# Kernel optimization log

Measured on AMD Instinct MI355X. Metric: run time of the kernel, lower is better.

## Reference

```python
import jax, jax.numpy as jnp
import numpy as np

H = 256  # rnn hidden size

def _rnn_dir(x, wih, whh, bih, bhh):
    # x: [B,T,D] -> outputs [B,T,H]; h_t = tanh(x_t Wih^T + bih + h_{t-1} Whh^T + bhh)
    xproj = jnp.einsum('btd,hd->bth', x, wih) + bih + bhh  # precompute input projection
    def step(h, xp):
        h = jnp.tanh(xp + h @ whh.T)
        return h, h
    h0 = jnp.zeros((x.shape[0], whh.shape[0]), x.dtype)
    _, ys = jax.lax.scan(step, h0, jnp.swapaxes(xproj, 0, 1))
    return jnp.swapaxes(ys, 0, 1)

def _birnn(x, wif, whf, bif, bhf, wib, whb, bib, bhb):
    fwd = _rnn_dir(x, wif, whf, bif, bhf)
    bwd = _rnn_dir(x[:, ::-1, :], wib, whb, bib, bhb)[:, ::-1, :]
    return jnp.concatenate([fwd, bwd], axis=-1)

def setup_inputs() -> dict:
    key = jax.random.key(0)
    ks = jax.random.split(key, 24)
    B, T, V, E = 64, 512, 131072, 128
    s = 0.05
    emb = jax.random.normal(ks[0], (V, E), jnp.float32) * s
    emb = emb.at[0].set(0.0)  # padding_idx=0
    def W(k, shp):
        return jax.random.normal(k, shp, jnp.float32) * s
    inp = {
        'x': jax.random.randint(ks[1], (B, T), 0, V),
        'emb': emb,
        'r1_wif': W(ks[2], (H, E)), 'r1_whf': W(ks[3], (H, H)),
        'r1_bif': W(ks[4], (H,)), 'r1_bhf': W(ks[5], (H,)),
        'r1_wib': W(ks[6], (H, E)), 'r1_whb': W(ks[7], (H, H)),
        'r1_bib': W(ks[8], (H,)), 'r1_bhb': W(ks[9], (H,)),
        'r2_wif': W(ks[10], (H, 2 * H)), 'r2_whf': W(ks[11], (H, H)),
        'r2_bif': W(ks[12], (H,)), 'r2_bhf': W(ks[13], (H,)),
        'r2_wib': W(ks[14], (H, 2 * H)), 'r2_whb': W(ks[15], (H, H)),
        'r2_bib': W(ks[16], (H,)), 'r2_bhb': W(ks[17], (H,)),
        'ln_g': jnp.ones((1024,), jnp.float32),
        'ln_b': jnp.zeros((1024,), jnp.float32),
        'w1': W(ks[18], (512, 1024)), 'b1': W(ks[19], (512,)),
        'w2': W(ks[20], (256, 512)), 'b2': W(ks[21], (256,)),
    }
    return inp

def reference(x, emb, r1_wif, r1_whf, r1_bif, r1_bhf, r1_wib, r1_whb, r1_bib, r1_bhb,
              r2_wif, r2_whf, r2_bif, r2_bhf, r2_wib, r2_whb, r2_bib, r2_bhb,
              ln_g, ln_b, w1, b1, w2, b2):
    e = emb[x]  # [B,T,128]
    o1 = _birnn(e, r1_wif, r1_whf, r1_bif, r1_bhf, r1_wib, r1_whb, r1_bib, r1_bhb)  # [B,T,512]
    o2 = _birnn(o1, r2_wif, r2_whf, r2_bif, r2_bhf, r2_wib, r2_whb, r2_bib, r2_bhb)  # [B,T,512]
    last = o2[:, -1, :]
    mean = jnp.mean(o2, axis=1)
    h = jnp.concatenate([last, mean], axis=1)  # [B,1024]
    mu = jnp.mean(h, axis=-1, keepdims=True)
    var = jnp.mean(jnp.square(h - mu), axis=-1, keepdims=True)
    h = (h - mu) * jax.lax.rsqrt(var + 1e-5) * ln_g + ln_b
    h = jax.nn.relu(h @ w1.T + b1)
    return h @ w2.T + b2
```

## Files before the change

### kernel.cpp

```cpp
#include <hip/hip_runtime.h>
#include <stdint.h>

typedef unsigned short u16;
typedef unsigned int   u32;
typedef __attribute__((ext_vector_type(8))) short short8;
typedef __attribute__((ext_vector_type(4))) float f32x4;

#define T_LEN 512
#define HID   256

__device__ __forceinline__ float bflo(u32 u){ union{u32 i; float f;} v; v.i = u << 16; return v.f; }
__device__ __forceinline__ float bfhi(u32 u){ union{u32 i; float f;} v; v.i = u & 0xffff0000u; return v.f; }
__device__ __forceinline__ float b2f(u16 s){ union{u32 i; float f;} v; v.i = ((u32)s) << 16; return v.f; }
__device__ __forceinline__ u16 f2b(float f){
  union{float f; u32 i;} v; v.f = f;
  u32 r = v.i + 0x7fffu + ((v.i >> 16) & 1u);
  return (u16)(r >> 16);
}
__device__ __forceinline__ u32 pk2(float a, float b){ return (u32)f2b(a) | ((u32)f2b(b) << 16); }
__device__ __forceinline__ float tanh_fast(float x){
  float ax = fabsf(x);
  float e  = __expf(-2.f * ax);
  float t  = (1.f - e) * __builtin_amdgcn_rcpf(1.f + e);
  return copysignf(t, x);
}
__device__ __forceinline__ bool flag_bf16(const u32* f){ return (f[0] & 0xFFFFu) == 0x3F80u; }

#define NT 22
struct ConvArgs {
  const void* src[NT];
  u32 off[NT];
  u32 total;
  const u32* flagsrc;
};

__global__ __launch_bounds__(256)
void convert_params(ConvArgs a, u16* __restrict__ dst)
{
  const bool bf = flag_bf16(a.flagsrc);
  const u32 stride = gridDim.x * blockDim.x;
  for (u32 g = blockIdx.x * blockDim.x + threadIdx.x; g < a.total; g += stride) {
    int t = 0;
    #pragma unroll
    for (int i = 1; i < NT; ++i) t += (g >= a.off[i]);
    u32 local = g - a.off[t];
    dst[g] = bf ? ((const u16*)a.src[t])[local]
                : f2b(((const float*)a.src[t])[local]);
  }
}

template<int K, int SRC>
__global__ __launch_bounds__(256, 2)
void wgemm(const void* Bsrc, const int* __restrict__ gidx,
           const u16* __restrict__ Wf, const u16* __restrict__ Wb,
           const u16* __restrict__ bif, const u16* __restrict__ bhf,
           const u16* __restrict__ bib, const u16* __restrict__ bhb,
           u16* outT, const u32* flagsrc)
{
  __shared__ __align__(16) u16 lds[64 * K];
  const int tid  = threadIdx.x;
  const int row0 = blockIdx.x * 64;
  const int bb   = row0 >> 9;
  const int t0   = row0 & 511;
  const int bt   = bb >> 4, nb = bb & 15;
  constexpr int CPR = K / 8;

  bool abf = true;
  if (SRC == 0) abf = flag_bf16(flagsrc);

  for (int i = tid; i < 64 * CPR; i += 256) {
    int r = i / CPR, c = i % CPR;
    uint4 v;
    if (SRC == 0) {
      long rb = (long)gidx[row0 + r] * K;
      if (abf) {
        v = *(const uint4*)((const u16*)Bsrc + rb + c * 8);
      } else {
        const float* af = (const float*)Bsrc;
        float4 lo = *(const float4*)(af + rb + c * 8);
        float4 hi = *(const float4*)(af + rb + c * 8 + 4);
        v.x = pk2(lo.x, lo.y); v.y = pk2(lo.z, lo.w);
        v.z = pk2(hi.x, hi.y); v.w = pk2(hi.z, hi.w);
      }
    } else {
      int k = c * 8, d = k >> 8;
      size_t e = (size_t)(d * 4 + bt) * 2097152 + (size_t)(t0 + r) * 4096
               + (size_t)nb * 256 + (k & 255);
      v = *(const uint4*)((const u16*)Bsrc + e);
    }
    *(uint4*)&lds[r * K + ((c ^ (r & 7)) * 8)] = v;
  }
  __syncthreads();

  const int w = tid >> 6, lane = tid & 63, n16 = lane & 15, quad = lane >> 4;
  const int d = w >> 1;
  const u16* W  = d ? Wb : Wf;
  const u16* bi = d ? bib : bif;
  const u16* bh = d ? bhb : bhf;
  const int mbase = (w & 1) * 128;

  f32x4 acc[8][4];
  #pragma unroll
  for (int i = 0; i < 8; ++i)
    #pragma unroll
    for (int j = 0; j < 4; ++j) acc[i][j] = (f32x4){0.f, 0.f, 0.f, 0.f};

  #pragma unroll
  for (int kk = 0; kk < K / 32; ++kk) {
    short8 bfr[4];
    #pragma unroll
    for (int j = 0; j < 4; ++j) {
      int r = j * 16 + n16;
      int c = (kk * 4 + quad) ^ (r & 7);
      bfr[j] = *(const short8*)&lds[r * K + c * 8];
    }
    #pragma unroll
    for (int i = 0; i < 8; ++i) {
      short8 afr = *(const short8*)(W + (size_t)(mbase + i * 16 + n16) * K + kk * 32 + quad * 8);
      #pragma unroll
      for (int j = 0; j < 4; ++j)
        acc[i][j] = __builtin_amdgcn_mfma_f32_16x16x32_bf16(afr, bfr[j], acc[i][j], 0, 0, 0);
    }
  }

  #pragma unroll
  for (int i = 0; i < 8; ++i) {
    int mrow0 = mbase + i * 16 + quad * 4;
    uint2 biv = *(const uint2*)(bi + mrow0);
    uint2 bhv = *(const uint2*)(bh + mrow0);
    float bias0 = b2f(biv.x & 0xffff) + b2f(bhv.x & 0xffff);
    float bias1 = b2f(biv.x >> 16)    + b2f(bhv.x >> 16);
    float bias2 = b2f(biv.y & 0xffff) + b2f(bhv.y & 0xffff);
    float bias3 = b2f(biv.y >> 16)    + b2f(bhv.y >> 16);
    #pragma unroll
    for (int j = 0; j < 4; ++j) {
      int t = t0 + j * 16 + n16;
      uint2 pv;
      pv.x = pk2(acc[i][j][0] + bias0, acc[i][j][1] + bias1);
      pv.y = pk2(acc[i][j][2] + bias2, acc[i][j][3] + bias3);
      size_t e = (size_t)(d * 4 + bt) * 2097152 + (size_t)t * 4096
               + (size_t)nb * 256 + mrow0;
      *(uint2*)(outT + e) = pv;
    }
  }
}

template<int MODE>
__device__ __forceinline__ void scan_step(
    int s, int dir, int n16, int quad, int m0,
    const u16 (&hrd)[16][264], u16 (&hwr)[16][264],
    uint2& pf,
    const u16* xptr, u16* optr,
    const short8 (&wa)[8], f32x4& sum, float* lastb, int lbase)
{
  const int t = dir ? (511 - s) : s;
  const uint2 xv = pf;
  {
    int s2 = (s + 2 < 512) ? s + 2 : 511;
    int t2 = dir ? (511 - s2) : s2;
    pf = *(const uint2*)(xptr + (size_t)t2 * 4096);
  }

  short8 hb[8];
  #pragma unroll
  for (int kk = 0; kk < 8; ++kk)
    hb[kk] = *(const short8*)&hrd[n16][kk * 32 + quad * 8];

  f32x4 acc0 = (f32x4){0.f, 0.f, 0.f, 0.f};
  f32x4 acc1 = (f32x4){0.f, 0.f, 0.f, 0.f};
  #pragma unroll
  for (int kk = 0; kk < 4; ++kk) {
    acc0 = __builtin_amdgcn_mfma_f32_16x16x32_bf16(wa[kk],     hb[kk],     acc0, 0, 0, 0);
    acc1 = __builtin_amdgcn_mfma_f32_16x16x32_bf16(wa[kk + 4], hb[kk + 4], acc1, 0, 0, 0);
  }

  float h0 = tanh_fast(acc0[0] + acc1[0] + b2f(xv.x & 0xffff));
  float h1 = tanh_fast(acc0[1] + acc1[1] + b2f(xv.x >> 16));
  float h2 = tanh_fast(acc0[2] + acc1[2] + b2f(xv.y & 0xffff));
  float h3 = tanh_fast(acc0[3] + acc1[3] + b2f(xv.y >> 16));
  uint2 hv; hv.x = pk2(h0, h1); hv.y = pk2(h2, h3);
  *(uint2*)&hwr[n16][m0] = hv;

  if (MODE == 0) {
    *(uint2*)(optr + (size_t)t * 4096) = hv;
  } else {
    sum += (f32x4){h0, h1, h2, h3};
    if (s == (dir ? 0 : 511))
      *(float4*)&lastb[(size_t)lbase] = (float4){h0, h1, h2, h3};
  }
  __syncthreads();
}

template<int MODE>
__global__ __launch_bounds__(1024)
void rnn_scan(const u16* xpT,
              const u16* __restrict__ whhF, const u16* __restrict__ whhB,
              u16* o1T, float* __restrict__ lastb, float* __restrict__ sumb)
{
  __shared__ __align__(16) u16 hl[2][16][264];
  const int tid = threadIdx.x, w = tid >> 6, lane = tid & 63;
  const int n16 = lane & 15, quad = lane >> 4;
  const int dir = blockIdx.x >> 2, bt = blockIdx.x & 3;
  const u16* whh = dir ? whhB : whhF;
  const int m0 = w * 16 + quad * 4;

  short8 wa[8];
  #pragma unroll
  for (int kk = 0; kk < 8; ++kk)
    wa[kk] = *(const short8*)(whh + (size_t)(w * 16 + n16) * 256 + kk * 32 + quad * 8);

  for (int i = tid; i < 16 * 264; i += 1024) ((u16*)hl[0])[i] = 0;

  const size_t blkbase = (size_t)(dir * 4 + bt) * 2097152;
  const u16* xptr = xpT + blkbase + (size_t)n16 * 256 + m0;
  u16*       optr = o1T + blkbase + (size_t)n16 * 256 + m0;
  const int lbase = (dir * 64 + bt * 16 + n16) * 256 + m0;

  uint2 pf0, pf1;
  {
    int ta = dir ? 511 : 0, tb = dir ? 510 : 1;
    pf0 = *(const uint2*)(xptr + (size_t)ta * 4096);
    pf1 = *(const uint2*)(xptr + (size_t)tb * 4096);
  }
  f32x4 sum = (f32x4){0.f, 0.f, 0.f, 0.f};
  __syncthreads();

  for (int s = 0; s < 512; s += 2) {
    scan_step<MODE>(s,     dir, n16, quad, m0, hl[0], hl[1], pf0, xptr, optr, wa, sum, lastb, lbase);
    scan_step<MODE>(s + 1, dir, n16, quad, m0, hl[1], hl[0], pf1, xptr, optr, wa, sum, lastb, lbase);
  }

  if (MODE == 1)
    *(float4*)&sumb[(size_t)lbase] = (float4){sum[0], sum[1], sum[2], sum[3]};
}

__device__ __forceinline__ float dot8(uint4 q, const float* hp){
  return bflo(q.x)*hp[0] + bfhi(q.x)*hp[1] + bflo(q.y)*hp[2] + bfhi(q.y)*hp[3]
       + bflo(q.z)*hp[4] + bfhi(q.z)*hp[5] + bflo(q.w)*hp[6] + bfhi(q.w)*hp[7];
}

__global__ __launch_bounds__(256)
void head_kernel(const float* __restrict__ lastb, const float* __restrict__ sumb,
                 const u16* __restrict__ g, const u16* __restrict__ be,
                 const u16* __restrict__ w1, const u16* __restrict__ b1,
                 const u16* __restrict__ w2, const u16* __restrict__ b2,
                 void* outv, const u32* flagsrc)
{
  __shared__ __align__(16) float hv[1024];
  __shared__ __align__(16) float act[512];
  __shared__ float red[8];
  const int tid = threadIdx.x;
  const int b   = blockIdx.x;
  const bool bf = flag_bf16(flagsrc);

  float v0 = lastb[b * 256 + tid];
  float v1 = lastb[(64 + b) * 256 + tid];
  float v2 = sumb[b * 256 + tid] * (1.f / 512.f);
  float v3 = sumb[(64 + b) * 256 + tid] * (1.f / 512.f);
  hv[tid] = v0; hv[256 + tid] = v1; hv[512 + tid] = v2; hv[768 + tid] = v3;

  float s  = v0 + v1 + v2 + v3;
  float ss = v0*v0 + v1*v1 + v2*v2 + v3*v3;
  #pragma unroll
  for (int off = 32; off; off >>= 1) {
    s  += __shfl_down(s, off);
    ss += __shfl_down(ss, off);
  }
  if ((tid & 63) == 0) { red[tid >> 6] = s; red[4 + (tid >> 6)] = ss; }
  __syncthreads();
  float S  = red[0] + red[1] + red[2] + red[3];
  float SS = red[4] + red[5] + red[6] + red[7];
  float mu   = S * (1.f / 1024.f);
  float var  = SS * (1.f / 1024.f) - mu * mu;
  float rstd = rsqrtf(var + 1e-5f);

  #pragma unroll
  for (int i = 0; i < 4; ++i) {
    int idx = i * 256 + tid;
    hv[idx] = (hv[idx] - mu) * rstd * b2f(g[idx]) + b2f(be[idx]);
  }
  __syncthreads();

  #pragma unroll
  for (int jj = 0; jj < 2; ++jj) {
    int j = jj * 256 + tid;
    const uint4* wr = (const uint4*)(w1 + (long)j * 1024);
    float a = 0.f;
    for (int c = 0; c < 128; ++c) a += dot8(wr[c], &hv[c * 8]);
    a += b2f(b1[j]);
    act[j] = a > 0.f ? a : 0.f;
  }
  __syncthreads();

  const uint4* wr2 = (const uint4*)(w2 + (long)tid * 512);
  float a = 0.f;
  for (int c = 0; c < 64; ++c) a += dot8(wr2[c], &act[c * 8]);
  a += b2f(b2[tid]);

  if (bf) {
    ((u16*)outv)[b * 256 + tid] = f2b(a);
  } else {
    union { u32 i; float f; } u; u.i = ((u32)f2b(a)) << 16;
    ((float*)outv)[b * 256 + tid] = u.f;
  }
}

extern "C" void kernel_launch(void* const* d_in, const int* in_sizes, int n_in,
                              void* d_out, int out_size, void* d_ws, size_t ws_size,
                              hipStream_t stream)
{
  const int* x    = (const int*)d_in[0];
  const u32* flag = (const u32*)d_in[18];

  static const int sizes[NT] = {
    32768, 65536, 256, 256, 32768, 65536, 256, 256,
    131072, 65536, 256, 256, 131072, 65536, 256, 256,
    1024, 1024, 524288, 512, 131072, 256
  };
  ConvArgs ca;
  u32 off = 0;
  for (int i = 0; i < NT; ++i) {
    ca.src[i] = d_in[2 + i];
    ca.off[i] = off;
    off += (u32)sizes[i];
  }
  ca.total = off;
  ca.flagsrc = flag;

  char* ws = (char*)d_ws;
  u16*   buf    = (u16*)ws;
  u16*   pm     = (u16*)(ws + 33554432);
  float* lastb  = (float*)(ws + 36054528);
  float* sumb   = (float*)(ws + 36185600);

  const u16* p_r1wif = pm + 0;
  const u16* p_r1whf = pm + 32768;
  const u16* p_r1bif = pm + 98304;
  const u16* p_r1bhf = pm + 98560;
  const u16* p_r1wib = pm + 98816;
  const u16* p_r1whb = pm + 131584;
  const u16* p_r1bib = pm + 197120;
  const u16* p_r1bhb = pm + 197376;
  const u16* p_r2wif = pm + 197632;
  const u16* p_r2whf = pm + 328704;
  const u16* p_r2bif = pm + 394240;
  const u16* p_r2bhf = pm + 394496;
  const u16* p_r2wib = pm + 394752;
  const u16* p_r2whb = pm + 525824;
  const u16* p_r2bib = pm + 591360;
  const u16* p_r2bhb = pm + 591616;
  const u16* p_lng   = pm + 591872;
  const u16* p_lnb   = pm + 592896;
  const u16* p_w1    = pm + 593920;
  const u16* p_b1    = pm + 1118208;
  const u16* p_w2    = pm + 1118720;
  const u16* p_b2    = pm + 1249792;

  convert_params<<<1024, 256, 0, stream>>>(ca, pm);

  wgemm<128, 0><<<512, 256, 0, stream>>>(d_in[1], x,
      p_r1wif, p_r1wib, p_r1bif, p_r1bhf, p_r1bib, p_r1bhb, buf, flag);
  rnn_scan<0><<<8, 1024, 0, stream>>>(buf, p_r1whf, p_r1whb, buf, nullptr, nullptr);
  wgemm<512, 1><<<512, 256, 0, stream>>>(buf, nullptr,
      p_r2wif, p_r2wib, p_r2bif, p_r2bhf, p_r2bib, p_r2bhb, buf, flag);
  rnn_scan<1><<<8, 1024, 0, stream>>>(buf, p_r2whf, p_r2whb, nullptr, lastb, sumb);
  head_kernel<<<64, 256, 0, stream>>>(lastb, sumb, p_lng, p_lnb, p_w1, p_b1, p_w2, p_b2,
      d_out, flag);
}
```

Before: 1.058 ms.

## Shrink RNN scan to 4 waves with 4 row-tiles each and cheaper barrier

```diff
diff --git a/kernel.cpp b/kernel.cpp
--- a/kernel.cpp
+++ b/kernel.cpp
@@ -18,11 +18,16 @@
   return (u16)(r >> 16);
 }
 __device__ __forceinline__ u32 pk2(float a, float b){ return (u32)f2b(a) | ((u32)f2b(b) << 16); }
-__device__ __forceinline__ float tanh_fast(float x){
-  float ax = fabsf(x);
-  float e  = __expf(-2.f * ax);
-  float t  = (1.f - e) * __builtin_amdgcn_rcpf(1.f + e);
-  return copysignf(t, x);
+__device__ __forceinline__ u32 cvtpk(float a, float b){
+  u32 r; asm("v_cvt_pk_bf16_f32 %0, %1, %2" : "=v"(r) : "v"(a), "v"(b)); return r;
+}
+__device__ __forceinline__ float tanh_c(float x){
+#if __has_builtin(__builtin_amdgcn_exp2f)
+  float e = __builtin_amdgcn_exp2f(x * 2.885390081777927f);
+#else
+  float e = __expf(x + x);
+#endif
+  return __builtin_fmaf(-2.f, __builtin_amdgcn_rcpf(e + 1.f), 1.f);
 }
 __device__ __forceinline__ bool flag_bf16(const u32* f){ return (f[0] & 0xFFFFu) == 0x3F80u; }
 
@@ -146,53 +151,59 @@
 }
 
 template<int MODE>
-__device__ __forceinline__ void scan_step(
-    int s, int dir, int n16, int quad, int m0,
-    const u16 (&hrd)[16][264], u16 (&hwr)[16][264],
-    uint2& pf,
-    const u16* xptr, u16* optr,
-    const short8 (&wa)[8], f32x4& sum, float* lastb, int lbase)
-{
-  const int t = dir ? (511 - s) : s;
-  const uint2 xv = pf;
-  {
-    int s2 = (s + 2 < 512) ? s + 2 : 511;
-    int t2 = dir ? (511 - s2) : s2;
-    pf = *(const uint2*)(xptr + (size_t)t2 * 4096);
-  }
+__device__ __forceinline__ void scan_step3(
+    int s, int send,
+    const u16* hrp,
+    u16* hwp,
+    uint2 (&pf)[4],
+    const u16*& xptr, u16*& optr, int pstep,
+    const short8 (&wa)[4][8], f32x4 (&sum)[4], float* lastb, int lbase)
+{
+  uint2 xv[4];
+  #pragma unroll
+  for (int j = 0; j < 4; ++j) xv[j] = pf[j];
+  #pragma unroll
+  for (int j = 0; j < 4; ++j) pf[j] = *(const uint2*)(xptr + j * 16);
+  xptr += pstep;
 
   short8 hb[8];
   #pragma unroll
   for (int kk = 0; kk < 8; ++kk)
-    hb[kk] = *(const short8*)&hrd[n16][kk * 32 + quad * 8];
-
-  f32x4 acc0 = (f32x4){0.f, 0.f, 0.f, 0.f};
-  f32x4 acc1 = (f32x4){0.f, 0.f, 0.f, 0.f};
-  #pragma unroll
-  for (int kk = 0; kk < 4; ++kk) {
-    acc0 = __builtin_amdgcn_mfma_f32_16x16x32_bf16(wa[kk],     hb[kk],     acc0, 0, 0, 0);
-    acc1 = __builtin_amdgcn_mfma_f32_16x16x32_bf16(wa[kk + 4], hb[kk + 4], acc1, 0, 0, 0);
-  }
-
-  float h0 = tanh_fast(acc0[0] + acc1[0] + b2f(xv.x & 0xffff));
-  float h1 = tanh_fast(acc0[1] + acc1[1] + b2f(xv.x >> 16));
-  float h2 = tanh_fast(acc0[2] + acc1[2] + b2f(xv.y & 0xffff));
-  float h3 = tanh_fast(acc0[3] + acc1[3] + b2f(xv.y >> 16));
-  uint2 hv; hv.x = pk2(h0, h1); hv.y = pk2(h2, h3);
-  *(uint2*)&hwr[n16][m0] = hv;
-
-  if (MODE == 0) {
-    *(uint2*)(optr + (size_t)t * 4096) = hv;
-  } else {
-    sum += (f32x4){h0, h1, h2, h3};
-    if (s == (dir ? 0 : 511))
-      *(float4*)&lastb[(size_t)lbase] = (float4){h0, h1, h2, h3};
-  }
-  __syncthreads();
+    hb[kk] = *(const short8*)(hrp + kk * 32);
+
+  f32x4 acc[4];
+  #pragma unroll
+  for (int j = 0; j < 4; ++j)
+    acc[j] = (f32x4){bflo(xv[j].x), bfhi(xv[j].x), bflo(xv[j].y), bfhi(xv[j].y)};
+  #pragma unroll
+  for (int kk = 0; kk < 8; ++kk)
+    #pragma unroll
+    for (int j = 0; j < 4; ++j)
+      acc[j] = __builtin_amdgcn_mfma_f32_16x16x32_bf16(wa[j][kk], hb[kk], acc[j], 0, 0, 0);
+
+  #pragma unroll
+  for (int j = 0; j < 4; ++j) {
+    float h0 = tanh_c(acc[j][0]), h1 = tanh_c(acc[j][1]);
+    float h2 = tanh_c(acc[j][2]), h3 = tanh_c(acc[j][3]);
+    uint2 hv; hv.x = cvtpk(h0, h1); hv.y = cvtpk(h2, h3);
+    *(uint2*)(hwp + j * 16) = hv;
+    if (MODE == 0) {
+      *(uint2*)(optr + j * 16) = hv;
+    } else {
+      sum[j] += (f32x4){h0, h1, h2, h3};
+      if (s == send)
+        *(float4*)&lastb[lbase + j * 16] = (float4){h0, h1, h2, h3};
+    }
+  }
+  if (MODE == 0) optr += pstep;
+
+  asm volatile("s_waitcnt lgkmcnt(0)" ::: "memory");
+  __builtin_amdgcn_s_barrier();
+  asm volatile("" ::: "memory");
 }
 
 template<int MODE>
-__global__ __launch_bounds__(1024)
+__global__ __launch_bounds__(256, 1)
 void rnn_scan(const u16* xpT,
               const u16* __restrict__ whhF, const u16* __restrict__ whhB,
               u16* o1T, float* __restrict__ lastb, float* __restrict__ sumb)
@@ -202,36 +213,53 @@
   const int n16 = lane & 15, quad = lane >> 4;
   const int dir = blockIdx.x >> 2, bt = blockIdx.x & 3;
   const u16* whh = dir ? whhB : whhF;
-  const int m0 = w * 16 + quad * 4;
-
-  short8 wa[8];
-  #pragma unroll
-  for (int kk = 0; kk < 8; ++kk)
-    wa[kk] = *(const short8*)(whh + (size_t)(w * 16 + n16) * 256 + kk * 32 + quad * 8);
-
-  for (int i = tid; i < 16 * 264; i += 1024) ((u16*)hl[0])[i] = 0;
+
+  short8 wa[4][8];
+  #pragma unroll
+  for (int j = 0; j < 4; ++j)
+    #pragma unroll
+    for (int kk = 0; kk < 8; ++kk)
+      wa[j][kk] = *(const short8*)(whh + (size_t)(w * 64 + j * 16 + n16) * 256
+                                       + kk * 32 + quad * 8);
+
+  for (int i = tid; i < 16 * 264; i += 256) ((u16*)hl[0])[i] = 0;
 
   const size_t blkbase = (size_t)(dir * 4 + bt) * 2097152;
-  const u16* xptr = xpT + blkbase + (size_t)n16 * 256 + m0;
-  u16*       optr = o1T + blkbase + (size_t)n16 * 256 + m0;
-  const int lbase = (dir * 64 + bt * 16 + n16) * 256 + m0;
-
-  uint2 pf0, pf1;
-  {
-    int ta = dir ? 511 : 0, tb = dir ? 510 : 1;
-    pf0 = *(const uint2*)(xptr + (size_t)ta * 4096);
-    pf1 = *(const uint2*)(xptr + (size_t)tb * 4096);
-  }
-  f32x4 sum = (f32x4){0.f, 0.f, 0.f, 0.f};
+  const int t0    = dir ? 511 : 0;
+  const int pstep = dir ? -4096 : 4096;
+  const u16* xptr = xpT + blkbase + (size_t)t0 * 4096 + n16 * 256 + w * 64 + quad * 4;
+  u16*       optr = o1T + blkbase + (size_t)t0 * 4096 + n16 * 256 + w * 64 + quad * 4;
+  const int lbase = (dir * 64 + bt * 16 + n16) * 256 + w * 64 + quad * 4;
+  const int send  = dir ? 0 : 511;
+
+  const u16* hr0 = &hl[0][n16][quad * 8];
+  const u16* hr1 = &hl[1][n16][quad * 8];
+  u16* hw0 = &hl[1][n16][w * 64 + quad * 4];
+  u16* hw1 = &hl[0][n16][w * 64 + quad * 4];
+
+  uint2 pf0[4], pf1[4];
+  #pragma unroll
+  for (int j = 0; j < 4; ++j) pf0[j] = *(const uint2*)(xptr + j * 16);
+  xptr += pstep;
+  #pragma unroll
+  for (int j = 0; j < 4; ++j) pf1[j] = *(const uint2*)(xptr + j * 16);
+  xptr += pstep;
+
+  f32x4 sum[4];
+  #pragma unroll
+  for (int j = 0; j < 4; ++j) sum[j] = (f32x4){0.f, 0.f, 0.f, 0.f};
   __syncthreads();
 
   for (int s = 0; s < 512; s += 2) {
-    scan_step<MODE>(s,     dir, n16, quad, m0, hl[0], hl[1], pf0, xptr, optr, wa, sum, lastb, lbase);
-    scan_step<MODE>(s + 1, dir, n16, quad, m0, hl[1], hl[0], pf1, xptr, optr, wa, sum, lastb, lbase);
-  }
-
-  if (MODE == 1)
-    *(float4*)&sumb[(size_t)lbase] = (float4){sum[0], sum[1], sum[2], sum[3]};
+    scan_step3<MODE>(s,     send, hr0, hw0, pf0, xptr, optr, pstep, wa, sum, lastb, lbase);
+    scan_step3<MODE>(s + 1, send, hr1, hw1, pf1, xptr, optr, pstep, wa, sum, lastb, lbase);
+  }
+
+  if (MODE == 1) {
+    #pragma unroll
+    for (int j = 0; j < 4; ++j)
+      *(float4*)&sumb[lbase + j * 16] = (float4){sum[j][0], sum[j][1], sum[j][2], sum[j][3]};
+  }
 }
 
 __device__ __forceinline__ float dot8(uint4 q, const float* hp){
@@ -360,10 +388,10 @@
 
   wgemm<128, 0><<<512, 256, 0, stream>>>(d_in[1], x,
       p_r1wif, p_r1wib, p_r1bif, p_r1bhf, p_r1bib, p_r1bhb, buf, flag);
-  rnn_scan<0><<<8, 1024, 0, stream>>>(buf, p_r1whf, p_r1whb, buf, nullptr, nullptr);
+  rnn_scan<0><<<8, 256, 0, stream>>>(buf, p_r1whf, p_r1whb, buf, nullptr, nullptr);
   wgemm<512, 1><<<512, 256, 0, stream>>>(buf, nullptr,
       p_r2wif, p_r2wib, p_r2bif, p_r2bhf, p_r2bib, p_r2bhb, buf, flag);
-  rnn_scan<1><<<8, 1024, 0, stream>>>(buf, p_r2whf, p_r2whb, nullptr, lastb, sumb);
+  rnn_scan<1><<<8, 256, 0, stream>>>(buf, p_r2whf, p_r2whb, nullptr, lastb, sumb);
   head_kernel<<<64, 256, 0, stream>>>(lastb, sumb, p_lng, p_lnb, p_w1, p_b1, p_w2, p_b2,
       d_out, flag);
 }
```

Result: slower. 1.127 ms (+6.5%).

## Prescale recurrent weights and projections to shorten tanh in RNN scan

Applied to the files above, without the earlier changes.

```diff
diff --git a/kernel.cpp b/kernel.cpp
--- a/kernel.cpp
+++ b/kernel.cpp
@@ -8,6 +8,7 @@
 
 #define T_LEN 512
 #define HID   256
+#define C2LE 2.8853900817779268f
 
 __device__ __forceinline__ float bflo(u32 u){ union{u32 i; float f;} v; v.i = u << 16; return v.f; }
 __device__ __forceinline__ float bfhi(u32 u){ union{u32 i; float f;} v; v.i = u & 0xffff0000u; return v.f; }
@@ -18,11 +19,16 @@
   return (u16)(r >> 16);
 }
 __device__ __forceinline__ u32 pk2(float a, float b){ return (u32)f2b(a) | ((u32)f2b(b) << 16); }
-__device__ __forceinline__ float tanh_fast(float x){
-  float ax = fabsf(x);
-  float e  = __expf(-2.f * ax);
-  float t  = (1.f - e) * __builtin_amdgcn_rcpf(1.f + e);
-  return copysignf(t, x);
+__device__ __forceinline__ u32 cvtpk(float a, float b){
+  u32 r; asm("v_cvt_pk_bf16_f32 %0, %1, %2" : "=v"(r) : "v"(a), "v"(b)); return r;
+}
+__device__ __forceinline__ float tanh_pre(float y){
+#if __has_builtin(__builtin_amdgcn_exp2f)
+  float e = __builtin_amdgcn_exp2f(y);
+#else
+  float e = exp2f(y);
+#endif
+  return __builtin_fmaf(-2.f, __builtin_amdgcn_rcpf(e + 1.f), 1.f);
 }
 __device__ __forceinline__ bool flag_bf16(const u32* f){ return (f[0] & 0xFFFFu) == 0x3F80u; }
 
@@ -44,8 +50,10 @@
     #pragma unroll
     for (int i = 1; i < NT; ++i) t += (g >= a.off[i]);
     u32 local = g - a.off[t];
-    dst[g] = bf ? ((const u16*)a.src[t])[local]
-                : f2b(((const float*)a.src[t])[local]);
+    float v = bf ? b2f(((const u16*)a.src[t])[local])
+                 : ((const float*)a.src[t])[local];
+    if (t == 1 || t == 5 || t == 9 || t == 13) v *= C2LE;
+    dst[g] = f2b(v);
   }
 }
 
@@ -136,8 +144,8 @@
     for (int j = 0; j < 4; ++j) {
       int t = t0 + j * 16 + n16;
       uint2 pv;
-      pv.x = pk2(acc[i][j][0] + bias0, acc[i][j][1] + bias1);
-      pv.y = pk2(acc[i][j][2] + bias2, acc[i][j][3] + bias3);
+      pv.x = cvtpk(C2LE * (acc[i][j][0] + bias0), C2LE * (acc[i][j][1] + bias1));
+      pv.y = cvtpk(C2LE * (acc[i][j][2] + bias2), C2LE * (acc[i][j][3] + bias3));
       size_t e = (size_t)(d * 4 + bt) * 2097152 + (size_t)t * 4096
                + (size_t)nb * 256 + mrow0;
       *(uint2*)(outT + e) = pv;
@@ -146,53 +154,54 @@
 }
 
 template<int MODE>
-__device__ __forceinline__ void scan_step(
-    int s, int dir, int n16, int quad, int m0,
-    const u16 (&hrd)[16][264], u16 (&hwr)[16][264],
+__device__ __forceinline__ void scan_step5(
+    int s, int send,
+    const u16* hrp,
+    u16* hwp,
     uint2& pf,
-    const u16* xptr, u16* optr,
+    const u16*& xptr, u16*& optr, int pstep,
     const short8 (&wa)[8], f32x4& sum, float* lastb, int lbase)
 {
-  const int t = dir ? (511 - s) : s;
-  const uint2 xv = pf;
-  {
-    int s2 = (s + 2 < 512) ? s + 2 : 511;
-    int t2 = dir ? (511 - s2) : s2;
-    pf = *(const uint2*)(xptr + (size_t)t2 * 4096);
-  }
-
   short8 hb[8];
   #pragma unroll
   for (int kk = 0; kk < 8; ++kk)
-    hb[kk] = *(const short8*)&hrd[n16][kk * 32 + quad * 8];
-
-  f32x4 acc0 = (f32x4){0.f, 0.f, 0.f, 0.f};
-  f32x4 acc1 = (f32x4){0.f, 0.f, 0.f, 0.f};
-  #pragma unroll
-  for (int kk = 0; kk < 4; ++kk) {
-    acc0 = __builtin_amdgcn_mfma_f32_16x16x32_bf16(wa[kk],     hb[kk],     acc0, 0, 0, 0);
-    acc1 = __builtin_amdgcn_mfma_f32_16x16x32_bf16(wa[kk + 4], hb[kk + 4], acc1, 0, 0, 0);
-  }
-
-  float h0 = tanh_fast(acc0[0] + acc1[0] + b2f(xv.x & 0xffff));
-  float h1 = tanh_fast(acc0[1] + acc1[1] + b2f(xv.x >> 16));
-  float h2 = tanh_fast(acc0[2] + acc1[2] + b2f(xv.y & 0xffff));
-  float h3 = tanh_fast(acc0[3] + acc1[3] + b2f(xv.y >> 16));
-  uint2 hv; hv.x = pk2(h0, h1); hv.y = pk2(h2, h3);
-  *(uint2*)&hwr[n16][m0] = hv;
+    hb[kk] = *(const short8*)(hrp + kk * 32);
+
+  uint2 xv = pf;
+  pf = *(const uint2*)(xptr);
+  xptr += pstep;
+
+  f32x4 a = (f32x4){bflo(xv.x), bfhi(xv.x), bflo(xv.y), bfhi(xv.y)};
+  f32x4 b = (f32x4){0.f, 0.f, 0.f, 0.f};
+  #pragma unroll
+  for (int kk = 0; kk < 8; kk += 2) {
+    a = __builtin_amdgcn_mfma_f32_16x16x32_bf16(wa[kk],     hb[kk],     a, 0, 0, 0);
+    b = __builtin_amdgcn_mfma_f32_16x16x32_bf16(wa[kk + 1], hb[kk + 1], b, 0, 0, 0);
+  }
+
+  float h0 = tanh_pre(a[0] + b[0]);
+  float h1 = tanh_pre(a[1] + b[1]);
+  float h2 = tanh_pre(a[2] + b[2]);
+  float h3 = tanh_pre(a[3] + b[3]);
+  uint2 hv; hv.x = cvtpk(h0, h1); hv.y = cvtpk(h2, h3);
+  *(uint2*)(hwp) = hv;
 
   if (MODE == 0) {
-    *(uint2*)(optr + (size_t)t * 4096) = hv;
+    *(uint2*)(optr) = hv;
+    optr += pstep;
   } else {
     sum += (f32x4){h0, h1, h2, h3};
-    if (s == (dir ? 0 : 511))
-      *(float4*)&lastb[(size_t)lbase] = (float4){h0, h1, h2, h3};
-  }
-  __syncthreads();
+    if (s == send)
+      *(float4*)&lastb[lbase] = (float4){h0, h1, h2, h3};
+  }
+
+  asm volatile("s_waitcnt lgkmcnt(0)" ::: "memory");
+  __builtin_amdgcn_s_barrier();
+  asm volatile("" ::: "memory");
 }
 
 template<int MODE>
-__global__ __launch_bounds__(1024)
+__global__ __launch_bounds__(1024, 4)
 void rnn_scan(const u16* xpT,
               const u16* __restrict__ whhF, const u16* __restrict__ whhB,
               u16* o1T, float* __restrict__ lastb, float* __restrict__ sumb)
@@ -212,26 +221,32 @@
   for (int i = tid; i < 16 * 264; i += 1024) ((u16*)hl[0])[i] = 0;
 
   const size_t blkbase = (size_t)(dir * 4 + bt) * 2097152;
-  const u16* xptr = xpT + blkbase + (size_t)n16 * 256 + m0;
-  u16*       optr = o1T + blkbase + (size_t)n16 * 256 + m0;
+  const int t0    = dir ? 511 : 0;
+  const int pstep = dir ? -4096 : 4096;
+  const u16* xptr = xpT + blkbase + (size_t)t0 * 4096 + n16 * 256 + m0;
+  u16*       optr = o1T + blkbase + (size_t)t0 * 4096 + n16 * 256 + m0;
   const int lbase = (dir * 64 + bt * 16 + n16) * 256 + m0;
+  const int send  = dir ? 0 : 511;
+
+  const u16* hr0 = &hl[0][n16][quad * 8];
+  const u16* hr1 = &hl[1][n16][quad * 8];
+  u16* hw0 = &hl[1][n16][m0];
+  u16* hw1 = &hl[0][n16][m0];
 
   uint2 pf0, pf1;
-  {
-    int ta = dir ? 511 : 0, tb = dir ? 510 : 1;
-    pf0 = *(const uint2*)(xptr + (size_t)ta * 4096);
-    pf1 = *(const uint2*)(xptr + (size_t)tb * 4096);
-  }
+  pf0 = *(const uint2*)(xptr); xptr += pstep;
+  pf1 = *(const uint2*)(xptr); xptr += pstep;
+
   f32x4 sum = (f32x4){0.f, 0.f, 0.f, 0.f};
   __syncthreads();
 
   for (int s = 0; s < 512; s += 2) {
-    scan_step<MODE>(s,     dir, n16, quad, m0, hl[0], hl[1], pf0, xptr, optr, wa, sum, lastb, lbase);
-    scan_step<MODE>(s + 1, dir, n16, quad, m0, hl[1], hl[0], pf1, xptr, optr, wa, sum, lastb, lbase);
+    scan_step5<MODE>(s,     send, hr0, hw0, pf0, xptr, optr, pstep, wa, sum, lastb, lbase);
+    scan_step5<MODE>(s + 1, send, hr1, hw1, pf1, xptr, optr, pstep, wa, sum, lastb, lbase);
   }
 
   if (MODE == 1)
-    *(float4*)&sumb[(size_t)lbase] = (float4){sum[0], sum[1], sum[2], sum[3]};
+    *(float4*)&sumb[lbase] = (float4){sum[0], sum[1], sum[2], sum[3]};
 }
 
 __device__ __forceinline__ float dot8(uint4 q, const float* hp){
```

Result: faster. 948.6 us (-10.4%).
